# Performance work log

Measured on AMD Instinct MI355X. Metric: run time of the kernel, lower is better.

Reference implementation:

```python
import jax, jax.numpy as jnp
import numpy as np

N_T, N_M, E, Q = 100000, 20000, 600000, 200000
F_IN, D, L = 256, 128, 2


def setup_inputs() -> dict:
    key = jax.random.key(0)
    ks = jax.random.split(key, 20)
    s = 1.0 / np.sqrt(D)
    inp = {
        "x_thesis": jax.random.normal(ks[0], (N_T, F_IN), jnp.float32),
        "mentor_node_id": jnp.arange(N_M, dtype=jnp.int64) if jax.config.jax_enable_x64 else jnp.arange(N_M, dtype=jnp.int32),
        "edge_src": jax.random.randint(ks[1], (E,), 0, N_T),
        "edge_dst": jax.random.randint(ks[2], (E,), 0, N_M),
        "eli_src": jax.random.randint(ks[3], (Q,), 0, N_T),
        "eli_dst": jax.random.randint(ks[4], (Q,), 0, N_M),
        # encoder params
        "thesis_lin_w": jax.random.normal(ks[5], (D, F_IN), jnp.float32) / np.sqrt(F_IN),
        "thesis_lin_b": jnp.zeros((D,), jnp.float32),
        "prof_emb": jax.random.normal(ks[6], (N_M, D), jnp.float32),
        # SAGEConv params per layer, per edge type (sup: thesis->mentor, rev: mentor->thesis)
        "W_nbr_sup": jax.random.normal(ks[7], (L, D, D), jnp.float32) * s,
        "W_root_sup": jax.random.normal(ks[8], (L, D, D), jnp.float32) * s,
        "b_sup": jnp.zeros((L, D), jnp.float32),
        "W_nbr_rev": jax.random.normal(ks[9], (L, D, D), jnp.float32) * s,
        "W_root_rev": jax.random.normal(ks[10], (L, D, D), jnp.float32) * s,
        "b_rev": jnp.zeros((L, D), jnp.float32),
        # classifier Linear(2*D -> 1)
        "cls_w": jax.random.normal(ks[11], (2 * D,), jnp.float32) * (1.0 / np.sqrt(2 * D)),
        "cls_b": jnp.zeros((), jnp.float32),
    }
    return inp


def reference(x_thesis, mentor_node_id, edge_src, edge_dst, eli_src, eli_dst,
              thesis_lin_w, thesis_lin_b, prof_emb,
              W_nbr_sup, W_root_sup, b_sup, W_nbr_rev, W_root_rev, b_rev,
              cls_w, cls_b):
    n_t = x_thesis.shape[0]
    n_m = prof_emb.shape[0]
    L_ = W_nbr_sup.shape[0]

    # node encoders
    h_t = x_thesis @ thesis_lin_w.T + thesis_lin_b          # [N_T, D]
    h_m = prof_emb[mentor_node_id]                          # [N_M, D]

    ones = jnp.ones(edge_src.shape[0], h_t.dtype)
    deg_m = jnp.maximum(jax.ops.segment_sum(ones, edge_dst, num_segments=n_m), 1.0)[:, None]
    deg_t = jnp.maximum(jax.ops.segment_sum(ones, edge_src, num_segments=n_t), 1.0)[:, None]

    for l in range(L_):
        # mean-aggregate thesis feats onto mentors (supervised_by edges)
        agg_m = jax.ops.segment_sum(h_t[edge_src], edge_dst, num_segments=n_m) / deg_m
        # mean-aggregate mentor feats onto theses (reverse edges)
        agg_t = jax.ops.segment_sum(h_m[edge_dst], edge_src, num_segments=n_t) / deg_t
        new_m = agg_m @ W_nbr_sup[l].T + h_m @ W_root_sup[l].T + b_sup[l]
        new_t = agg_t @ W_nbr_rev[l].T + h_t @ W_root_rev[l].T + b_rev[l]
        if l < L_ - 1:
            new_m = jax.nn.relu(new_m)
            new_t = jax.nn.relu(new_t)
        h_t, h_m = new_t, new_m

    # edge-level classifier: gather endpoints, concat, linear -> scalar per pair
    z = jnp.concatenate([h_t[eli_src], h_m[eli_dst]], axis=-1)  # [Q, 2D]
    return z @ cls_w + cls_b                                     # [Q]
```

## Files before the change

### kernel.cpp

```cpp
#include <hip/hip_runtime.h>
#include <cstdint>
#include <cstddef>

#define D 128
#define F_IN 256

typedef __attribute__((ext_vector_type(8))) short bf16x8;
typedef __attribute__((ext_vector_type(4))) float f32x4;

__device__ __forceinline__ unsigned short f2bs(float f) {
  unsigned int x = __builtin_bit_cast(unsigned int, f);
  x = x + 0x7fffu + ((x >> 16) & 1u);
  return (unsigned short)(x >> 16);
}
__device__ __forceinline__ float b2f(unsigned int lo16) {
  unsigned int x = lo16 << 16;
  return __builtin_bit_cast(float, x);
}
__device__ __forceinline__ void gl_lds16v(const void* g, void* l) {
  __builtin_amdgcn_global_load_lds(
      (__attribute__((address_space(1))) void*)g,
      (__attribute__((address_space(3))) void*)l, 16, 0, 0);
}
__device__ __forceinline__ uint4 pack8(float4 a, float4 b) {
  uint4 o;
  o.x = (unsigned)f2bs(a.x) | ((unsigned)f2bs(a.y) << 16);
  o.y = (unsigned)f2bs(a.z) | ((unsigned)f2bs(a.w) << 16);
  o.z = (unsigned)f2bs(b.x) | ((unsigned)f2bs(b.y) << 16);
  o.w = (unsigned)f2bs(b.z) | ((unsigned)f2bs(b.w) << 16);
  return o;
}


__global__ __launch_bounds__(256) void prep_k(
    const float* __restrict__ s0, unsigned short* __restrict__ d0, int n0,
    const float* __restrict__ s1, unsigned short* __restrict__ d1, int n1,
    const float* __restrict__ s2, unsigned short* __restrict__ d2, int n2,
    const float* __restrict__ s3, unsigned short* __restrict__ d3, int n3,
    const float* __restrict__ s4, unsigned short* __restrict__ d4, int n4,
    int nbC,
    const float* __restrict__ emb, const int* __restrict__ ids,
    unsigned short* __restrict__ hm, int NM, int nbG,
    const int* __restrict__ esrc, const int* __restrict__ edst,
    int* __restrict__ bktT, int* __restrict__ bktM,
    int E, int SHT, int SHM, int nbA)
{
  int bid = blockIdx.x;
  int tid = threadIdx.x;
  if (bid < nbC) {
    int j = bid * 256 + tid;
    const float* s; unsigned short* d;
    if (j < n0) { s = s0; d = d0; }
    else {
      j -= n0;
      if (j < n1) { s = s1; d = d1; }
      else {
        j -= n1;
        if (j < n2) { s = s2; d = d2; }
        else {
          j -= n2;
          if (j < n3) { s = s3; d = d3; }
          else { j -= n3; if (j >= n4) return; s = s4; d = d4; }
        }
      }
    }
    const float4* sp = (const float4*)(s + (size_t)j * 8);
    *(uint4*)(d + (size_t)j * 8) = pack8(sp[0], sp[1]);
    return;
  }
  bid -= nbC;
  if (bid < nbG) {
    int i = bid * 256 + tid;
    if (i >= NM * 16) return;
    int r = i >> 4, c = (i & 15) * 8;
    const float* s = emb + (size_t)ids[r] * D + c;
    *(uint4*)(hm + (size_t)r * D + c) = pack8(*(const float4*)s, *(const float4*)(s + 4));
    return;
  }
  bid -= nbG;
  __shared__ int sh[256];
  sh[tid] = 0;
  __syncthreads();
  int stride = nbA * 256;
  for (int e = bid * 256 + tid; e < E; e += stride) {
    atomicAdd(&sh[esrc[e] >> SHT], 1);
    atomicAdd(&sh[128 + (edst[e] >> SHM)], 1);
  }
  __syncthreads();
  if (tid < 128) { if (sh[tid]) atomicAdd(&bktT[tid], sh[tid]); }
  else { if (sh[tid]) atomicAdd(&bktM[tid - 128], sh[tid]); }
}


__global__ void a2_scan_k(const int* __restrict__ bktT, int* __restrict__ baseT, int* __restrict__ curT, int BT,
                          const int* __restrict__ bktM, int* __restrict__ baseM, int* __restrict__ curM, int BM) {
  __shared__ int sT[129], sM[129];
  int tid = threadIdx.x;
  if (tid < BT) sT[tid] = bktT[tid];
  if (tid < BM) sM[tid] = bktM[tid];
  __syncthreads();
  if (tid == 0) { int r = 0; for (int i = 0; i < BT; ++i) { int c = sT[i]; sT[i] = r; r += c; } sT[BT] = r; }
  if (tid == 1) { int r = 0; for (int i = 0; i < BM; ++i) { int c = sM[i]; sM[i] = r; r += c; } sM[BM] = r; }
  __syncthreads();
  if (tid <= BT) { baseT[tid] = sT[tid]; if (tid < BT) curT[tid] = sT[tid]; }
  if (tid <= BM) { baseM[tid] = sM[tid]; if (tid < BM) curM[tid] = sM[tid]; }
}


#define CH 4096

__global__ __launch_bounds__(256) void a3_part_k(
    const int* __restrict__ esrc, const int* __restrict__ edst,
    unsigned* __restrict__ partT, unsigned* __restrict__ partM,
    int* __restrict__ curT, int* __restrict__ curM,
    int E, int BT, int BM, int SHT, int SHM)
{
  __shared__ unsigned stT[CH], stM[CH];
  __shared__ int hT[128], lbT[128], lcT[128], gbT[128];
  __shared__ int hM[128], lbM[128], lcM[128], gbM[128];
  __shared__ int st2[256];
  int tid = threadIdx.x;
  int c0 = blockIdx.x * CH;
  int len = E - c0; if (len > CH) len = CH;

  if (tid < 128) { hT[tid] = 0; hM[tid] = 0; }
  __syncthreads();
  for (int i = tid; i < len; i += 256) {
    atomicAdd(&hT[esrc[c0 + i] >> SHT], 1);
    atomicAdd(&hM[edst[c0 + i] >> SHM], 1);
  }
  __syncthreads();
  int own = (tid < 128) ? hT[tid] : hM[tid - 128];
  st2[tid] = own;
  __syncthreads();
  for (int dd = 1; dd < 128; dd <<= 1) {
    int y = ((tid & 127) >= dd) ? st2[tid - dd] : 0;
    __syncthreads();
    st2[tid] += y;
    __syncthreads();
  }
  int excl = st2[tid] - own;
  if (tid < 128) { lbT[tid] = excl; lcT[tid] = excl; }
  else { lbM[tid - 128] = excl; lcM[tid - 128] = excl; }
  __syncthreads();
  if (tid < BT) { if (hT[tid]) gbT[tid] = atomicAdd(&curT[tid], hT[tid]); }
  if (tid >= 128 && tid - 128 < BM) { int m = tid - 128; if (hM[m]) gbM[m] = atomicAdd(&curM[m], hM[m]); }
  __syncthreads();
  for (int i = tid; i < len; i += 256) {
    unsigned s = (unsigned)esrc[c0 + i], dn = (unsigned)edst[c0 + i];
    int p = atomicAdd(&lcT[s >> SHT], 1);
    stT[p] = (s << 15) | dn;
    int q = atomicAdd(&lcM[dn >> SHM], 1);
    stM[q] = (dn << 17) | s;
  }
  __syncthreads();
  for (int b = 0; b < BT; ++b) {
    int cb = hT[b]; if (!cb) continue;
    int lb = lbT[b]; int gb = gbT[b];
    for (int i = tid; i < cb; i += 256) partT[gb + i] = stT[lb + i];
  }
  for (int b = 0; b < BM; ++b) {
    int cb = hM[b]; if (!cb) continue;
    int lb = lbM[b]; int gb = gbM[b];
    for (int i = tid; i < cb; i += 256) partM[gb + i] = stM[lb + i];
  }
}


#define BCAP 12288

__global__ __launch_bounds__(256) void b_csr_k(
    const unsigned* __restrict__ partT, const int* __restrict__ baseT,
    int* __restrict__ rowT, int* __restrict__ csrT, int NT, int BT, int SHT,
    const unsigned* __restrict__ partM, const int* __restrict__ baseM,
    int* __restrict__ rowM, int* __restrict__ csrM, int NM, int BM, int SHM, int E)
{
  __shared__ int cnt[1024];
  __shared__ int st[256];
  __shared__ unsigned stage[BCAP];

  const unsigned* part; const int* base; int* row; int* csr;
  int N, SH, KS; unsigned PM; int b; bool last;
  if ((int)blockIdx.x < BT) {
    part = partT; base = baseT; row = rowT; csr = csrT;
    N = NT; SH = SHT; KS = 15; PM = 0x7fffu; b = blockIdx.x; last = (b == BT - 1);
  } else {
    part = partM; base = baseM; row = rowM; csr = csrM;
    N = NM; SH = SHM; KS = 17; PM = 0x1ffffu; b = blockIdx.x - BT; last = (b == BM - 1);
  }
  int tid = threadIdx.x;
  int ebeg = base[b], eend = base[b + 1];
  int tot = eend - ebeg;
  int n0 = b << SH;
  int width = 1 << SH;
  int nw = N - n0; if (nw > width) nw = width;
  int seg = (width + 255) >> 8;

  for (int j = 0; j < seg; ++j) { int idx = tid * seg + j; if (idx < nw) cnt[idx] = 0; }
  __syncthreads();
  for (int i = tid; i < tot; i += 256) {
    int k = (int)(part[ebeg + i] >> KS) - n0;
    atomicAdd(&cnt[k], 1);
  }
  __syncthreads();
  int s = 0;
  for (int j = 0; j < seg; ++j) { int idx = tid * seg + j; if (idx < nw) s += cnt[idx]; }
  st[tid] = s;
  __syncthreads();
  for (int dd = 1; dd < 256; dd <<= 1) {
    int y = (tid >= dd) ? st[tid - dd] : 0;
    __syncthreads();
    st[tid] += y;
    __syncthreads();
  }
  int run = st[tid] - s;
  for (int j = 0; j < seg; ++j) {
    int idx = tid * seg + j;
    if (idx < nw) {
      int c = cnt[idx];
      row[n0 + idx] = ebeg + run;
      cnt[idx] = run;
      run += c;
    }
  }
  if (last && tid == 0) row[N] = E;
  __syncthreads();
  if (tot <= BCAP) {
    for (int i = tid; i < tot; i += 256) {
      unsigned p = part[ebeg + i];
      int k = (int)(p >> KS) - n0;
      int pos = atomicAdd(&cnt[k], 1);
      stage[pos] = p & PM;
    }
    __syncthreads();
    for (int i = tid; i < tot; i += 256) csr[ebeg + i] = (int)stage[i];
  } else {
    for (int i = tid; i < tot; i += 256) {
      unsigned p = part[ebeg + i];
      int k = (int)(p >> KS) - n0;
      int pos = atomicAdd(&cnt[k], 1);
      csr[ebeg + pos] = (int)(p & PM);
    }
  }
}


__global__ __launch_bounds__(256) void aggregate2_k(
    const unsigned short* __restrict__ tabM, const int* __restrict__ rowpM,
    const int* __restrict__ idxM, unsigned short* __restrict__ outM, int nM, int nblkM,
    const unsigned short* __restrict__ tabT, const int* __restrict__ rowpT,
    const int* __restrict__ idxT, unsigned short* __restrict__ outT, int nT)
{
  const unsigned short* tab; const int* rowp; const int* idx;
  unsigned short* outp; int n, nodeb;
  if ((int)blockIdx.x < nblkM) {
    tab = tabM; rowp = rowpM; idx = idxM; outp = outM; n = nM;
    nodeb = blockIdx.x * 8;
  } else {
    tab = tabT; rowp = rowpT; idx = idxT; outp = outT; n = nT;
    nodeb = (blockIdx.x - nblkM) * 8;
  }
  const int tid = threadIdx.x;
  const int l = tid & 63;
  const int l32 = l & 31;
  const int sub = l >> 5;
  const int node = nodeb + (tid >> 6) * 2 + sub;
  const int nodeC = node < n ? node : n - 1;
  int b = rowp[nodeC];
  int e = rowp[nodeC + 1];
  if (node >= n) e = b;
  const int deg = e - b;
  const int odeg = __shfl_xor(deg, 32, 64);
  const int trip = deg > odeg ? deg : odeg;
  const int qsafe = (e > b) ? (e - 1) : 0;
  const unsigned short* tl = tab + l32 * 4;
  float a0 = 0.f, a1 = 0.f, a2 = 0.f, a3 = 0.f;
  int k = 0;
  while (k + 8 <= trip) {
    int nn[8]; bool ok[8];
#pragma unroll
    for (int u = 0; u < 8; ++u) { int p = b + k + u; ok[u] = p < e; nn[u] = idx[ok[u] ? p : qsafe]; }
    uint2 vv[8];
#pragma unroll
    for (int u = 0; u < 8; ++u) { vv[u] = make_uint2(0u, 0u); if (ok[u]) vv[u] = *(const uint2*)(tl + (size_t)nn[u] * D); }
#pragma unroll
    for (int u = 0; u < 8; ++u) {
      a0 += b2f(vv[u].x & 0xffffu); a1 += b2f(vv[u].x >> 16);
      a2 += b2f(vv[u].y & 0xffffu); a3 += b2f(vv[u].y >> 16);
    }
    k += 8;
  }
  if (k + 4 <= trip) {
    int nn[4]; bool ok[4];
#pragma unroll
    for (int u = 0; u < 4; ++u) { int p = b + k + u; ok[u] = p < e; nn[u] = idx[ok[u] ? p : qsafe]; }
    uint2 vv[4];
#pragma unroll
    for (int u = 0; u < 4; ++u) { vv[u] = make_uint2(0u, 0u); if (ok[u]) vv[u] = *(const uint2*)(tl + (size_t)nn[u] * D); }
#pragma unroll
    for (int u = 0; u < 4; ++u) {
      a0 += b2f(vv[u].x & 0xffffu); a1 += b2f(vv[u].x >> 16);
      a2 += b2f(vv[u].y & 0xffffu); a3 += b2f(vv[u].y >> 16);
    }
    k += 4;
  }
  if (k < trip) {
    int nn[3]; bool ok[3];
#pragma unroll
    for (int u = 0; u < 3; ++u) { int p = b + k + u; ok[u] = p < e; nn[u] = idx[ok[u] ? p : qsafe]; }
    uint2 vv[3];
#pragma unroll
    for (int u = 0; u < 3; ++u) { vv[u] = make_uint2(0u, 0u); if (ok[u]) vv[u] = *(const uint2*)(tl + (size_t)nn[u] * D); }
#pragma unroll
    for (int u = 0; u < 3; ++u) {
      a0 += b2f(vv[u].x & 0xffffu); a1 += b2f(vv[u].x >> 16);
      a2 += b2f(vv[u].y & 0xffffu); a3 += b2f(vv[u].y >> 16);
    }
  }
  float inv = 1.0f / (float)(deg > 1 ? deg : 1);
  if (node < n) {
    uint2 o;
    o.x = (unsigned)f2bs(a0 * inv) | ((unsigned)f2bs(a1 * inv) << 16);
    o.y = (unsigned)f2bs(a2 * inv) | ((unsigned)f2bs(a3 * inv) << 16);
    *(uint2*)(outp + (size_t)node * D + l32 * 4) = o;
  }
}


template<bool RELU>
__device__ __forceinline__ void gemm_body(
    const unsigned short* __restrict__ Aop, const unsigned short* __restrict__ WA,
    const unsigned short* __restrict__ Bop, const unsigned short* __restrict__ WB,
    const float* __restrict__ bias, unsigned short* __restrict__ out, int M,
    int blk, char* smraw)
{
  unsigned short* bufA0 = (unsigned short*)smraw;
  unsigned short* bufW0 = (unsigned short*)(smraw + 16384);
  const int tid = threadIdx.x;
  const int w = tid >> 6, l = tid & 63;
  const int wr = w >> 1, wc = w & 1;
  const int lr = l & 15, kg = l >> 4;
  const int row0 = blk * 128;
  const int srow = l >> 2;
  const int su = l & 3;

  f32x4 acc[4][4] = {};

  auto stage = [&](int st, int bsel) {
    const unsigned short* Ap = (st < 4) ? Aop : Bop;
    const unsigned short* Wp = (st < 4) ? WA : WB;
    int k0 = (st & 3) * 32;
    unsigned short* bA = bufA0 + bsel * 4096;
    unsigned short* bW = bufW0 + bsel * 4096;
#pragma unroll
    for (int q = 0; q < 2; ++q) {
      int r = w * 32 + q * 16 + srow;
      int gr = row0 + r; if (gr >= M) gr = M - 1;
      int gu = su ^ ((r >> 1) & 3);
      gl_lds16v(Ap + (size_t)gr * D + k0 + gu * 8, bA + (w * 32 + q * 16) * 32 + l * 8);
      gl_lds16v(Wp + (size_t)r * D + k0 + gu * 8, bW + (w * 32 + q * 16) * 32 + l * 8);
    }
  };

  stage(0, 0);
#pragma unroll 1
  for (int st = 0; st < 8; ++st) {
    if (st < 7) {
      stage(st + 1, (st + 1) & 1);
      __builtin_amdgcn_sched_barrier(0);
      asm volatile("s_waitcnt vmcnt(4)" ::: "memory");
    } else {
      __builtin_amdgcn_sched_barrier(0);
      asm volatile("s_waitcnt vmcnt(0)" ::: "memory");
    }
    __builtin_amdgcn_s_barrier();
    __builtin_amdgcn_sched_barrier(0);
    const unsigned short* bA = bufA0 + (st & 1) * 4096;
    const unsigned short* bW = bufW0 + (st & 1) * 4096;
    bf16x8 aF[4], bF[4];
#pragma unroll
    for (int i = 0; i < 4; ++i) {
      int r = wr * 64 + i * 16 + lr;
      aF[i] = *(const bf16x8*)&bA[r * 32 + ((kg ^ ((r >> 1) & 3)) * 8)];
    }
#pragma unroll
    for (int j = 0; j < 4; ++j) {
      int r = wc * 64 + j * 16 + lr;
      bF[j] = *(const bf16x8*)&bW[r * 32 + ((kg ^ ((r >> 1) & 3)) * 8)];
    }
#pragma unroll
    for (int i = 0; i < 4; ++i)
#pragma unroll
      for (int j = 0; j < 4; ++j)
        acc[i][j] = __builtin_amdgcn_mfma_f32_16x16x32_bf16(aF[i], bF[j], acc[i][j], 0, 0, 0);
    __builtin_amdgcn_sched_barrier(0);
    __builtin_amdgcn_s_barrier();
  }

  __syncthreads();
  float bn[4];
#pragma unroll
  for (int j = 0; j < 4; ++j) bn[j] = bias[wc * 64 + j * 16 + lr];
  unsigned short* ow = (unsigned short*)smraw + w * 4096;
#pragma unroll
  for (int i = 0; i < 4; ++i)
#pragma unroll
    for (int j = 0; j < 4; ++j) {
      f32x4 v = acc[i][j];
#pragma unroll
      for (int r = 0; r < 4; ++r) {
        float x = v[r] + bn[j];
        if (RELU) x = fmaxf(x, 0.f);
        ow[(i * 16 + kg * 4 + r) * 64 + j * 16 + lr] = f2bs(x);
      }
    }
  __syncthreads();
#pragma unroll
  for (int q = 0; q < 8; ++q) {
    int u = q * 64 + l;
    int lrow = u >> 3;
    int cu = (u & 7) * 8;
    int gr = row0 + wr * 64 + lrow;
    if (gr < M)
      *(uint4*)(out + (size_t)gr * D + wc * 64 + cu) = *(const uint4*)&ow[lrow * 64 + cu];
  }
}

template<bool RELU>
__global__ __launch_bounds__(256) void gemm_pair_k(
    const unsigned short* __restrict__ Am, const unsigned short* __restrict__ WAm,
    const unsigned short* __restrict__ Bm, const unsigned short* __restrict__ WBm,
    const float* __restrict__ biasm, unsigned short* __restrict__ outm, int Mm, int nbm,
    const unsigned short* __restrict__ At, const unsigned short* __restrict__ WAt,
    const unsigned short* __restrict__ Bt, const unsigned short* __restrict__ WBt,
    const float* __restrict__ biast, unsigned short* __restrict__ outt, int Mt)
{
  __shared__ char smraw[32768];
  if ((int)blockIdx.x < nbm)
    gemm_body<RELU>(Am, WAm, Bm, WBm, biasm, outm, Mm, blockIdx.x, smraw);
  else
    gemm_body<RELU>(At, WAt, Bt, WBt, biast, outt, Mt, blockIdx.x - nbm, smraw);
}

__global__ __launch_bounds__(256) void gemm_enc_k(
    const float* __restrict__ A, const unsigned short* __restrict__ W,
    const float* __restrict__ bias, unsigned short* __restrict__ out, int M)
{
  __shared__ char smraw[49152];
  float* bufA0 = (float*)smraw;
  unsigned short* bufW0 = (unsigned short*)(smraw + 32768);
  const int tid = threadIdx.x;
  const int w = tid >> 6, l = tid & 63;
  const int wr = w >> 1, wc = w & 1;
  const int lr = l & 15, kg = l >> 4;
  const int row0 = blockIdx.x * 128;
  const int arow = l >> 3;
  const int au = l & 7;
  const int wrow = l >> 2;
  const int wu = l & 3;

  f32x4 acc[4][4] = {};

  auto stage = [&](int st, int bsel) {
    int k0 = st * 32;
    float* bA = bufA0 + bsel * 4096;
    unsigned short* bW = bufW0 + bsel * 4096;
#pragma unroll
    for (int q = 0; q < 4; ++q) {
      int r = w * 32 + q * 8 + arow;
      int gr = row0 + r; if (gr >= M) gr = M - 1;
      int gu = au ^ (r & 7);
      gl_lds16v(A + (size_t)gr * F_IN + k0 + gu * 4, bA + (w * 32 + q * 8) * 32 + l * 4);
    }
#pragma unroll
    for (int q = 0; q < 2; ++q) {
      int r = w * 32 + q * 16 + wrow;
      int gu = wu ^ ((r >> 1) & 3);
      gl_lds16v(W + (size_t)r * F_IN + k0 + gu * 8, bW + (w * 32 + q * 16) * 32 + l * 8);
    }
  };

  stage(0, 0);
#pragma unroll 1
  for (int st = 0; st < F_IN / 32; ++st) {
    if (st < F_IN / 32 - 1) {
      stage(st + 1, (st + 1) & 1);
      __builtin_amdgcn_sched_barrier(0);
      asm volatile("s_waitcnt vmcnt(6)" ::: "memory");
    } else {
      __builtin_amdgcn_sched_barrier(0);
      asm volatile("s_waitcnt vmcnt(0)" ::: "memory");
    }
    __builtin_amdgcn_s_barrier();
    __builtin_amdgcn_sched_barrier(0);
    const float* bA = bufA0 + (st & 1) * 4096;
    const unsigned short* bW = bufW0 + (st & 1) * 4096;
    bf16x8 aF[4], bF[4];
#pragma unroll
    for (int i = 0; i < 4; ++i) {
      int r = wr * 64 + i * 16 + lr;
      const float4* pa = (const float4*)(bA + r * 32);
      float4 v0 = pa[(2 * kg) ^ (r & 7)];
      float4 v1 = pa[(2 * kg + 1) ^ (r & 7)];
      uint4 c = pack8(v0, v1);
      aF[i] = *(bf16x8*)&c;
    }
#pragma unroll
    for (int j = 0; j < 4; ++j) {
      int r = wc * 64 + j * 16 + lr;
      bF[j] = *(const bf16x8*)&bW[r * 32 + ((kg ^ ((r >> 1) & 3)) * 8)];
    }
#pragma unroll
    for (int i = 0; i < 4; ++i)
#pragma unroll
      for (int j = 0; j < 4; ++j)
        acc[i][j] = __builtin_amdgcn_mfma_f32_16x16x32_bf16(aF[i], bF[j], acc[i][j], 0, 0, 0);
    __builtin_amdgcn_sched_barrier(0);
    __builtin_amdgcn_s_barrier();
  }

  __syncthreads();
  float bn[4];
#pragma unroll
  for (int j = 0; j < 4; ++j) bn[j] = bias[wc * 64 + j * 16 + lr];
  unsigned short* ow = (unsigned short*)smraw + w * 4096;
#pragma unroll
  for (int i = 0; i < 4; ++i)
#pragma unroll
    for (int j = 0; j < 4; ++j) {
      f32x4 v = acc[i][j];
#pragma unroll
      for (int r = 0; r < 4; ++r)
        ow[(i * 16 + kg * 4 + r) * 64 + j * 16 + lr] = f2bs(v[r] + bn[j]);
    }
  __syncthreads();
#pragma unroll
  for (int q = 0; q < 8; ++q) {
    int u = q * 64 + l;
    int lrow = u >> 3;
    int cu = (u & 7) * 8;
    int gr = row0 + wr * 64 + lrow;
    if (gr < M)
      *(uint4*)(out + (size_t)gr * D + wc * 64 + cu) = *(const uint4*)&ow[lrow * 64 + cu];
  }
}


__global__ __launch_bounds__(256) void classify_k(
    const unsigned short* __restrict__ ht, const unsigned short* __restrict__ hm,
    const int* __restrict__ qs, const int* __restrict__ qd,
    const float* __restrict__ w, const float* __restrict__ bptr,
    float* __restrict__ out, int Q)
{
  int g = blockIdx.x * 8 + (threadIdx.x >> 5);
  if (g >= Q) return;
  int l = threadIdx.x & 31;
  const unsigned short* src = (l < 16)
      ? ht + (size_t)qs[g] * D + l * 8
      : hm + (size_t)qd[g] * D + (l - 16) * 8;
  uint4 v = *(const uint4*)src;
  const float* wp = w + l * 8;
  float acc = 0.f;
  acc += b2f(v.x & 0xffffu) * wp[0];
  acc += b2f(v.x >> 16)     * wp[1];
  acc += b2f(v.y & 0xffffu) * wp[2];
  acc += b2f(v.y >> 16)     * wp[3];
  acc += b2f(v.z & 0xffffu) * wp[4];
  acc += b2f(v.z >> 16)     * wp[5];
  acc += b2f(v.w & 0xffffu) * wp[6];
  acc += b2f(v.w >> 16)     * wp[7];
#pragma unroll
  for (int m = 16; m >= 1; m >>= 1) acc += __shfl_xor(acc, m, 64);
  if (l == 0) out[g] = acc + bptr[0];
}


extern "C" void kernel_launch(void* const* d_in, const int* in_sizes, int n_in,
                              void* d_out, int out_size, void* d_ws, size_t ws_size,
                              hipStream_t stream)
{
  const float* x_thesis = (const float*)d_in[0];
  const int*   mentor_id = (const int*)d_in[1];
  const int*   esrc = (const int*)d_in[2];
  const int*   edst = (const int*)d_in[3];
  const int*   qsrc = (const int*)d_in[4];
  const int*   qdst = (const int*)d_in[5];
  const float* lin_w = (const float*)d_in[6];
  const float* lin_b = (const float*)d_in[7];
  const float* prof  = (const float*)d_in[8];
  const float* Wn_sup = (const float*)d_in[9];
  const float* Wr_sup = (const float*)d_in[10];
  const float* b_sup  = (const float*)d_in[11];
  const float* Wn_rev = (const float*)d_in[12];
  const float* Wr_rev = (const float*)d_in[13];
  const float* b_rev  = (const float*)d_in[14];
  const float* cls_w  = (const float*)d_in[15];
  const float* cls_b  = (const float*)d_in[16];

  const int NT = in_sizes[0] / F_IN;
  const int NM = in_sizes[1];
  const int E  = in_sizes[2];
  const int Q  = in_sizes[4];
  const int L  = in_sizes[11] / D;

  int SHT = 0; while ((((NT - 1) >> SHT) + 1) > 128) ++SHT;
  int SHM = 0; while ((((NM - 1) >> SHM) + 1) > 128) ++SHM;
  const int BT = ((NT - 1) >> SHT) + 1;
  const int BM = ((NM - 1) >> SHM) + 1;

  char* wsb = (char*)d_ws;
  size_t off = 0;
  auto alloc = [&](size_t bytes) {
    void* p = wsb + off;
    off = (off + bytes + 255) & ~(size_t)255;
    return p;
  };
  unsigned short* h_t   = (unsigned short*)alloc((size_t)NT * D * 2);
  unsigned short* a_t   = (unsigned short*)alloc((size_t)NT * D * 2);
  unsigned short* h_m   = (unsigned short*)alloc((size_t)NM * D * 2);
  unsigned short* a_m   = (unsigned short*)alloc((size_t)NM * D * 2);
  unsigned short* linw_bf = (unsigned short*)alloc((size_t)D * F_IN * 2);
  unsigned short* wns_bf  = (unsigned short*)alloc((size_t)L * D * D * 2);
  unsigned short* wrs_bf  = (unsigned short*)alloc((size_t)L * D * D * 2);
  unsigned short* wnr_bf  = (unsigned short*)alloc((size_t)L * D * D * 2);
  unsigned short* wrr_bf  = (unsigned short*)alloc((size_t)L * D * D * 2);
  int* row_t = (int*)alloc(((size_t)NT + 1) * 4);
  int* row_m = (int*)alloc(((size_t)NM + 1) * 4);
  int* csr_t = (int*)alloc((size_t)E * 4);
  int* csr_m = (int*)alloc((size_t)E * 4);
  unsigned* partT = (unsigned*)alloc((size_t)E * 4);
  unsigned* partM = (unsigned*)alloc((size_t)E * 4);
  size_t bkt_off = off;
  int* bktT  = (int*)alloc(128 * 4);
  int* bktM  = (int*)alloc(128 * 4);
  size_t bkt_end = off;
  int* baseT = (int*)alloc(129 * 4);
  int* baseM = (int*)alloc(129 * 4);
  int* curT  = (int*)alloc(128 * 4);
  int* curM  = (int*)alloc(128 * 4);
  (void)n_in; (void)out_size; (void)ws_size;

  (void)hipMemsetAsync(wsb + bkt_off, 0, bkt_end - bkt_off, stream);

  {
    int n0 = D * F_IN / 8, nw = L * D * D / 8;
    int totc = n0 + 4 * nw;
    int nbC = (totc + 255) / 256;
    int nbG = (NM * 16 + 255) / 256;
    int nbA = 256;
    prep_k<<<nbC + nbG + nbA, 256, 0, stream>>>(
        lin_w, linw_bf, n0, Wn_sup, wns_bf, nw, Wr_sup, wrs_bf, nw,
        Wn_rev, wnr_bf, nw, Wr_rev, wrr_bf, nw, nbC,
        prof, mentor_id, h_m, NM, nbG,
        esrc, edst, bktT, bktM, E, SHT, SHM, nbA);
  }
  a2_scan_k<<<1, 256, 0, stream>>>(bktT, baseT, curT, BT, bktM, baseM, curM, BM);
  a3_part_k<<<(E + CH - 1) / CH, 256, 0, stream>>>(
      esrc, edst, partT, partM, curT, curM, E, BT, BM, SHT, SHM);
  b_csr_k<<<BT + BM, 256, 0, stream>>>(
      partT, baseT, row_t, csr_t, NT, BT, SHT,
      partM, baseM, row_m, csr_m, NM, BM, SHM, E);

  gemm_enc_k<<<(NT + 127) / 128, 256, 0, stream>>>(x_thesis, linw_bf, lin_b, h_t, NT);

  int agg_nbm = (NM + 7) / 8, agg_nbt = (NT + 7) / 8;
  int gem_nbm = (NM + 127) / 128, gem_nbt = (NT + 127) / 128;
  for (int l = 0; l < L; ++l) {
    aggregate2_k<<<agg_nbm + agg_nbt, 256, 0, stream>>>(
        h_t, row_m, csr_m, a_m, NM, agg_nbm,
        h_m, row_t, csr_t, a_t, NT);

    const unsigned short* wns = wns_bf + (size_t)l * D * D;
    const unsigned short* wrs = wrs_bf + (size_t)l * D * D;
    const unsigned short* wnr = wnr_bf + (size_t)l * D * D;
    const unsigned short* wrr = wrr_bf + (size_t)l * D * D;
    const float* bs = b_sup + (size_t)l * D;
    const float* br = b_rev + (size_t)l * D;
    if (l < L - 1) {
      gemm_pair_k<true><<<gem_nbm + gem_nbt, 256, 0, stream>>>(
          a_m, wns, h_m, wrs, bs, a_m, NM, gem_nbm,
          a_t, wnr, h_t, wrr, br, a_t, NT);
    } else {
      gemm_pair_k<false><<<gem_nbm + gem_nbt, 256, 0, stream>>>(
          a_m, wns, h_m, wrs, bs, a_m, NM, gem_nbm,
          a_t, wnr, h_t, wrr, br, a_t, NT);
    }
    unsigned short* tmp;
    tmp = h_t; h_t = a_t; a_t = tmp;
    tmp = h_m; h_m = a_m; a_m = tmp;
  }

  classify_k<<<(Q + 7) / 8, 256, 0, stream>>>(h_t, h_m, qsrc, qdst, cls_w, cls_b,
                                              (float*)d_out, Q);
}
```

Before: 270.6 us.

## Fuse neighbor aggregation into per-layer SAGE GEMM kernel via LDS staging

Merges the separate aggregate kernel and the dual GEMM into one layer kernel. Each 64-row block first gathers and mean-reduces neighbor features into swizzled LDS, then runs the MFMA GEMM over the aggregate (from LDS) and the root features (streamed in). This removes the round trip of the aggregate through global memory and one launch per layer. In exchange the gather uses one 32-lane group per node, handled serially over 8 nodes, so per-node load-level parallelism drops. The GEMM also loses its double-buffered pipelining and the block tile shrinks to 64 rows.

```diff
diff --git a/kernel.cpp b/kernel.cpp
--- a/kernel.cpp
+++ b/kernel.cpp
@@ -13,6 +13,9 @@
   x = x + 0x7fffu + ((x >> 16) & 1u);
   return (unsigned short)(x >> 16);
 }
+__device__ __forceinline__ unsigned pk2(float lo, float hi) {
+  return (unsigned)f2bs(lo) | ((unsigned)f2bs(hi) << 16);
+}
 __device__ __forceinline__ float b2f(unsigned int lo16) {
   unsigned int x = lo16 << 16;
   return __builtin_bit_cast(float, x);
@@ -24,10 +27,8 @@
 }
 __device__ __forceinline__ uint4 pack8(float4 a, float4 b) {
   uint4 o;
-  o.x = (unsigned)f2bs(a.x) | ((unsigned)f2bs(a.y) << 16);
-  o.y = (unsigned)f2bs(a.z) | ((unsigned)f2bs(a.w) << 16);
-  o.z = (unsigned)f2bs(b.x) | ((unsigned)f2bs(b.y) << 16);
-  o.w = (unsigned)f2bs(b.z) | ((unsigned)f2bs(b.w) << 16);
+  o.x = pk2(a.x, a.y); o.y = pk2(a.z, a.w);
+  o.z = pk2(b.x, b.y); o.w = pk2(b.z, b.w);
   return o;
 }
 
@@ -245,165 +246,137 @@
 }
 
 
-__global__ __launch_bounds__(256) void aggregate2_k(
-    const unsigned short* __restrict__ tabM, const int* __restrict__ rowpM,
-    const int* __restrict__ idxM, unsigned short* __restrict__ outM, int nM, int nblkM,
-    const unsigned short* __restrict__ tabT, const int* __restrict__ rowpT,
-    const int* __restrict__ idxT, unsigned short* __restrict__ outT, int nT)
-{
-  const unsigned short* tab; const int* rowp; const int* idx;
-  unsigned short* outp; int n, nodeb;
-  if ((int)blockIdx.x < nblkM) {
-    tab = tabM; rowp = rowpM; idx = idxM; outp = outM; n = nM;
-    nodeb = blockIdx.x * 8;
-  } else {
-    tab = tabT; rowp = rowpT; idx = idxT; outp = outT; n = nT;
-    nodeb = (blockIdx.x - nblkM) * 8;
-  }
-  const int tid = threadIdx.x;
-  const int l = tid & 63;
-  const int l32 = l & 31;
-  const int sub = l >> 5;
-  const int node = nodeb + (tid >> 6) * 2 + sub;
-  const int nodeC = node < n ? node : n - 1;
-  int b = rowp[nodeC];
-  int e = rowp[nodeC + 1];
-  if (node >= n) e = b;
-  const int deg = e - b;
-  const int odeg = __shfl_xor(deg, 32, 64);
-  const int trip = deg > odeg ? deg : odeg;
-  const int qsafe = (e > b) ? (e - 1) : 0;
-  const unsigned short* tl = tab + l32 * 4;
-  float a0 = 0.f, a1 = 0.f, a2 = 0.f, a3 = 0.f;
-  int k = 0;
-  while (k + 8 <= trip) {
-    int nn[8]; bool ok[8];
-#pragma unroll
-    for (int u = 0; u < 8; ++u) { int p = b + k + u; ok[u] = p < e; nn[u] = idx[ok[u] ? p : qsafe]; }
-    uint2 vv[8];
-#pragma unroll
-    for (int u = 0; u < 8; ++u) { vv[u] = make_uint2(0u, 0u); if (ok[u]) vv[u] = *(const uint2*)(tl + (size_t)nn[u] * D); }
-#pragma unroll
-    for (int u = 0; u < 8; ++u) {
-      a0 += b2f(vv[u].x & 0xffffu); a1 += b2f(vv[u].x >> 16);
-      a2 += b2f(vv[u].y & 0xffffu); a3 += b2f(vv[u].y >> 16);
-    }
-    k += 8;
-  }
-  if (k + 4 <= trip) {
-    int nn[4]; bool ok[4];
-#pragma unroll
-    for (int u = 0; u < 4; ++u) { int p = b + k + u; ok[u] = p < e; nn[u] = idx[ok[u] ? p : qsafe]; }
-    uint2 vv[4];
-#pragma unroll
-    for (int u = 0; u < 4; ++u) { vv[u] = make_uint2(0u, 0u); if (ok[u]) vv[u] = *(const uint2*)(tl + (size_t)nn[u] * D); }
-#pragma unroll
-    for (int u = 0; u < 4; ++u) {
-      a0 += b2f(vv[u].x & 0xffffu); a1 += b2f(vv[u].x >> 16);
-      a2 += b2f(vv[u].y & 0xffffu); a3 += b2f(vv[u].y >> 16);
-    }
-    k += 4;
-  }
-  if (k < trip) {
-    int nn[3]; bool ok[3];
-#pragma unroll
-    for (int u = 0; u < 3; ++u) { int p = b + k + u; ok[u] = p < e; nn[u] = idx[ok[u] ? p : qsafe]; }
-    uint2 vv[3];
-#pragma unroll
-    for (int u = 0; u < 3; ++u) { vv[u] = make_uint2(0u, 0u); if (ok[u]) vv[u] = *(const uint2*)(tl + (size_t)nn[u] * D); }
-#pragma unroll
-    for (int u = 0; u < 3; ++u) {
-      a0 += b2f(vv[u].x & 0xffffu); a1 += b2f(vv[u].x >> 16);
-      a2 += b2f(vv[u].y & 0xffffu); a3 += b2f(vv[u].y >> 16);
-    }
-  }
-  float inv = 1.0f / (float)(deg > 1 ? deg : 1);
-  if (node < n) {
-    uint2 o;
-    o.x = (unsigned)f2bs(a0 * inv) | ((unsigned)f2bs(a1 * inv) << 16);
-    o.y = (unsigned)f2bs(a2 * inv) | ((unsigned)f2bs(a3 * inv) << 16);
-    *(uint2*)(outp + (size_t)node * D + l32 * 4) = o;
-  }
-}
-
-
 template<bool RELU>
-__device__ __forceinline__ void gemm_body(
-    const unsigned short* __restrict__ Aop, const unsigned short* __restrict__ WA,
-    const unsigned short* __restrict__ Bop, const unsigned short* __restrict__ WB,
-    const float* __restrict__ bias, unsigned short* __restrict__ out, int M,
-    int blk, char* smraw)
-{
-  unsigned short* bufA0 = (unsigned short*)smraw;
-  unsigned short* bufW0 = (unsigned short*)(smraw + 16384);
+__device__ __forceinline__ void layer_body(
+    const unsigned short* __restrict__ tab, const int* __restrict__ rowp,
+    const int* __restrict__ idx, const unsigned short* __restrict__ root,
+    const unsigned short* __restrict__ Wn, const unsigned short* __restrict__ Wr,
+    const float* __restrict__ bias, unsigned short* __restrict__ out,
+    int n, int blk, char* smraw)
+{
+  unsigned short* aggp = (unsigned short*)smraw;
+  unsigned short* wbuf = (unsigned short*)(smraw + 16384);
+  unsigned short* rbuf = (unsigned short*)(smraw + 24576);
   const int tid = threadIdx.x;
   const int w = tid >> 6, l = tid & 63;
+  const int g = tid >> 5;
+  const int l32 = tid & 31;
   const int wr = w >> 1, wc = w & 1;
   const int lr = l & 15, kg = l >> 4;
-  const int row0 = blk * 128;
-  const int srow = l >> 2;
-  const int su = l & 3;
-
-  f32x4 acc[4][4] = {};
-
-  auto stage = [&](int st, int bsel) {
-    const unsigned short* Ap = (st < 4) ? Aop : Bop;
-    const unsigned short* Wp = (st < 4) ? WA : WB;
-    int k0 = (st & 3) * 32;
-    unsigned short* bA = bufA0 + bsel * 4096;
-    unsigned short* bW = bufW0 + bsel * 4096;
-#pragma unroll
-    for (int q = 0; q < 2; ++q) {
-      int r = w * 32 + q * 16 + srow;
-      int gr = row0 + r; if (gr >= M) gr = M - 1;
-      int gu = su ^ ((r >> 1) & 3);
-      gl_lds16v(Ap + (size_t)gr * D + k0 + gu * 8, bA + (w * 32 + q * 16) * 32 + l * 8);
-      gl_lds16v(Wp + (size_t)r * D + k0 + gu * 8, bW + (w * 32 + q * 16) * 32 + l * 8);
-    }
-  };
-
-  stage(0, 0);
+  const int n0 = blk * 64;
+
+  const unsigned short* tl = tab + l32 * 4;
+  for (int i = 0; i < 8; ++i) {
+    int r = g * 8 + i;
+    int node = n0 + r;
+    int nodeC = node < n ? node : n - 1;
+    int b = rowp[nodeC];
+    int e = rowp[nodeC + 1];
+    if (node >= n) e = b;
+    int deg = e - b;
+    float a0 = 0.f, a1 = 0.f, a2 = 0.f, a3 = 0.f;
+    int p = b;
+    while (p + 8 <= e) {
+      int nn[8];
+#pragma unroll
+      for (int u = 0; u < 8; ++u) nn[u] = idx[p + u];
+      uint2 vv[8];
+#pragma unroll
+      for (int u = 0; u < 8; ++u) vv[u] = *(const uint2*)(tl + (size_t)nn[u] * D);
+#pragma unroll
+      for (int u = 0; u < 8; ++u) {
+        a0 += b2f(vv[u].x & 0xffffu); a1 += b2f(vv[u].x >> 16);
+        a2 += b2f(vv[u].y & 0xffffu); a3 += b2f(vv[u].y >> 16);
+      }
+      p += 8;
+    }
+    if (p + 4 <= e) {
+      int nn[4];
+#pragma unroll
+      for (int u = 0; u < 4; ++u) nn[u] = idx[p + u];
+      uint2 vv[4];
+#pragma unroll
+      for (int u = 0; u < 4; ++u) vv[u] = *(const uint2*)(tl + (size_t)nn[u] * D);
+#pragma unroll
+      for (int u = 0; u < 4; ++u) {
+        a0 += b2f(vv[u].x & 0xffffu); a1 += b2f(vv[u].x >> 16);
+        a2 += b2f(vv[u].y & 0xffffu); a3 += b2f(vv[u].y >> 16);
+      }
+      p += 4;
+    }
+    {
+      bool h0 = p < e, h1 = p + 1 < e, h2 = p + 2 < e;
+      int m0 = h0 ? idx[p] : 0, m1 = h1 ? idx[p + 1] : 0, m2 = h2 ? idx[p + 2] : 0;
+      uint2 w0 = make_uint2(0u, 0u), w1 = make_uint2(0u, 0u), w2 = make_uint2(0u, 0u);
+      if (h0) w0 = *(const uint2*)(tl + (size_t)m0 * D);
+      if (h1) w1 = *(const uint2*)(tl + (size_t)m1 * D);
+      if (h2) w2 = *(const uint2*)(tl + (size_t)m2 * D);
+      if (h0) { a0 += b2f(w0.x & 0xffffu); a1 += b2f(w0.x >> 16); a2 += b2f(w0.y & 0xffffu); a3 += b2f(w0.y >> 16); }
+      if (h1) { a0 += b2f(w1.x & 0xffffu); a1 += b2f(w1.x >> 16); a2 += b2f(w1.y & 0xffffu); a3 += b2f(w1.y >> 16); }
+      if (h2) { a0 += b2f(w2.x & 0xffffu); a1 += b2f(w2.x >> 16); a2 += b2f(w2.y & 0xffffu); a3 += b2f(w2.y >> 16); }
+    }
+    float inv = 1.0f / (float)(deg > 1 ? deg : 1);
+    int u = (l32 >> 1) ^ (r & 7);
+    *(uint2*)(aggp + r * 128 + u * 8 + (l32 & 1) * 4) =
+        make_uint2(pk2(a0 * inv, a1 * inv), pk2(a2 * inv, a3 * inv));
+  }
+  __syncthreads();
+
+  f32x4 acc[2][4] = {};
+  const int srow = l >> 2, su = l & 3;
 #pragma unroll 1
-  for (int st = 0; st < 8; ++st) {
-    if (st < 7) {
-      stage(st + 1, (st + 1) & 1);
-      __builtin_amdgcn_sched_barrier(0);
-      asm volatile("s_waitcnt vmcnt(4)" ::: "memory");
+  for (int ch = 0; ch < 8; ++ch) {
+    if (ch) __syncthreads();
+    {
+      const unsigned short* Wp = (ch < 4) ? Wn : Wr;
+      int k0 = (ch & 3) * 32;
+#pragma unroll
+      for (int q = 0; q < 2; ++q) {
+        int r = w * 32 + q * 16 + srow;
+        int gu = su ^ ((r >> 1) & 3);
+        gl_lds16v(Wp + (size_t)r * D + k0 + gu * 8, wbuf + (w * 32 + q * 16) * 32 + l * 8);
+      }
+      if (ch >= 4) {
+        int r = tid >> 2;
+        int gr = n0 + r; if (gr >= n) gr = n - 1;
+        int gu = su ^ ((r >> 1) & 3);
+        gl_lds16v(root + (size_t)gr * D + k0 + gu * 8, rbuf + r * 32 + su * 8);
+      }
+    }
+    __syncthreads();
+    bf16x8 aF[2], bF[4];
+    if (ch < 4) {
+#pragma unroll
+      for (int i = 0; i < 2; ++i) {
+        int rr = wr * 32 + i * 16 + lr;
+        int u = ((ch & 3) * 4 + kg) ^ (rr & 7);
+        aF[i] = *(const bf16x8*)&aggp[rr * 128 + u * 8];
+      }
     } else {
-      __builtin_amdgcn_sched_barrier(0);
-      asm volatile("s_waitcnt vmcnt(0)" ::: "memory");
-    }
-    __builtin_amdgcn_s_barrier();
-    __builtin_amdgcn_sched_barrier(0);
-    const unsigned short* bA = bufA0 + (st & 1) * 4096;
-    const unsigned short* bW = bufW0 + (st & 1) * 4096;
-    bf16x8 aF[4], bF[4];
-#pragma unroll
-    for (int i = 0; i < 4; ++i) {
-      int r = wr * 64 + i * 16 + lr;
-      aF[i] = *(const bf16x8*)&bA[r * 32 + ((kg ^ ((r >> 1) & 3)) * 8)];
+#pragma unroll
+      for (int i = 0; i < 2; ++i) {
+        int rr = wr * 32 + i * 16 + lr;
+        aF[i] = *(const bf16x8*)&rbuf[rr * 32 + ((kg ^ ((rr >> 1) & 3)) * 8)];
+      }
     }
 #pragma unroll
     for (int j = 0; j < 4; ++j) {
       int r = wc * 64 + j * 16 + lr;
-      bF[j] = *(const bf16x8*)&bW[r * 32 + ((kg ^ ((r >> 1) & 3)) * 8)];
-    }
-#pragma unroll
-    for (int i = 0; i < 4; ++i)
+      bF[j] = *(const bf16x8*)&wbuf[r * 32 + ((kg ^ ((r >> 1) & 3)) * 8)];
+    }
+#pragma unroll
+    for (int i = 0; i < 2; ++i)
 #pragma unroll
       for (int j = 0; j < 4; ++j)
         acc[i][j] = __builtin_amdgcn_mfma_f32_16x16x32_bf16(aF[i], bF[j], acc[i][j], 0, 0, 0);
-    __builtin_amdgcn_sched_barrier(0);
-    __builtin_amdgcn_s_barrier();
   }
 
   __syncthreads();
   float bn[4];
 #pragma unroll
   for (int j = 0; j < 4; ++j) bn[j] = bias[wc * 64 + j * 16 + lr];
-  unsigned short* ow = (unsigned short*)smraw + w * 4096;
-#pragma unroll
-  for (int i = 0; i < 4; ++i)
+#pragma unroll
+  for (int i = 0; i < 2; ++i)
 #pragma unroll
     for (int j = 0; j < 4; ++j) {
       f32x4 v = acc[i][j];
@@ -411,36 +384,39 @@
       for (int r = 0; r < 4; ++r) {
         float x = v[r] + bn[j];
         if (RELU) x = fmaxf(x, 0.f);
-        ow[(i * 16 + kg * 4 + r) * 64 + j * 16 + lr] = f2bs(x);
-      }
-    }
-  __syncthreads();
-#pragma unroll
-  for (int q = 0; q < 8; ++q) {
-    int u = q * 64 + l;
-    int lrow = u >> 3;
-    int cu = (u & 7) * 8;
-    int gr = row0 + wr * 64 + lrow;
-    if (gr < M)
-      *(uint4*)(out + (size_t)gr * D + wc * 64 + cu) = *(const uint4*)&ow[lrow * 64 + cu];
+        aggp[(wr * 32 + i * 16 + kg * 4 + r) * 128 + wc * 64 + j * 16 + lr] = f2bs(x);
+      }
+    }
+  __syncthreads();
+#pragma unroll
+  for (int q = 0; q < 4; ++q) {
+    int u = q * 256 + tid;
+    int lrow = u >> 4;
+    int cu = (u & 15) * 8;
+    int gr = n0 + lrow;
+    if (gr < n)
+      *(uint4*)(out + (size_t)gr * D + cu) = *(const uint4*)&aggp[lrow * 128 + cu];
   }
 }
 
 template<bool RELU>
-__global__ __launch_bounds__(256) void gemm_pair_k(
-    const unsigned short* __restrict__ Am, const unsigned short* __restrict__ WAm,
-    const unsigned short* __restrict__ Bm, const unsigned short* __restrict__ WBm,
-    const float* __restrict__ biasm, unsigned short* __restrict__ outm, int Mm, int nbm,
-    const unsigned short* __restrict__ At, const unsigned short* __restrict__ WAt,
-    const unsigned short* __restrict__ Bt, const unsigned short* __restrict__ WBt,
-    const float* __restrict__ biast, unsigned short* __restrict__ outt, int Mt)
-{
-  __shared__ char smraw[32768];
+__global__ __launch_bounds__(256) void layer_k(
+    const unsigned short* __restrict__ tabM, const int* __restrict__ rowpM,
+    const int* __restrict__ idxM, const unsigned short* __restrict__ rootM,
+    const unsigned short* __restrict__ WnM, const unsigned short* __restrict__ WrM,
+    const float* __restrict__ biasM, unsigned short* __restrict__ outM, int nM, int nbm,
+    const unsigned short* __restrict__ tabT, const int* __restrict__ rowpT,
+    const int* __restrict__ idxT, const unsigned short* __restrict__ rootT,
+    const unsigned short* __restrict__ WnT, const unsigned short* __restrict__ WrT,
+    const float* __restrict__ biasT, unsigned short* __restrict__ outT, int nT)
+{
+  __shared__ char smraw[28672];
   if ((int)blockIdx.x < nbm)
-    gemm_body<RELU>(Am, WAm, Bm, WBm, biasm, outm, Mm, blockIdx.x, smraw);
+    layer_body<RELU>(tabM, rowpM, idxM, rootM, WnM, WrM, biasM, outM, nM, blockIdx.x, smraw);
   else
-    gemm_body<RELU>(At, WAt, Bt, WBt, biast, outt, Mt, blockIdx.x - nbm, smraw);
-}
+    layer_body<RELU>(tabT, rowpT, idxT, rootT, WnT, WrT, biasT, outT, nT, blockIdx.x - nbm, smraw);
+}
+
 
 __global__ __launch_bounds__(256) void gemm_enc_k(
     const float* __restrict__ A, const unsigned short* __restrict__ W,
@@ -663,13 +639,8 @@
 
   gemm_enc_k<<<(NT + 127) / 128, 256, 0, stream>>>(x_thesis, linw_bf, lin_b, h_t, NT);
 
-  int agg_nbm = (NM + 7) / 8, agg_nbt = (NT + 7) / 8;
-  int gem_nbm = (NM + 127) / 128, gem_nbt = (NT + 127) / 128;
+  int nbm64 = (NM + 63) / 64, nbt64 = (NT + 63) / 64;
   for (int l = 0; l < L; ++l) {
-    aggregate2_k<<<agg_nbm + agg_nbt, 256, 0, stream>>>(
-        h_t, row_m, csr_m, a_m, NM, agg_nbm,
-        h_m, row_t, csr_t, a_t, NT);
-
     const unsigned short* wns = wns_bf + (size_t)l * D * D;
     const unsigned short* wrs = wrs_bf + (size_t)l * D * D;
     const unsigned short* wnr = wnr_bf + (size_t)l * D * D;
@@ -677,13 +648,13 @@
     const float* bs = b_sup + (size_t)l * D;
     const float* br = b_rev + (size_t)l * D;
     if (l < L - 1) {
-      gemm_pair_k<true><<<gem_nbm + gem_nbt, 256, 0, stream>>>(
-          a_m, wns, h_m, wrs, bs, a_m, NM, gem_nbm,
-          a_t, wnr, h_t, wrr, br, a_t, NT);
+      layer_k<true><<<nbm64 + nbt64, 256, 0, stream>>>(
+          h_t, row_m, csr_m, h_m, wns, wrs, bs, a_m, NM, nbm64,
+          h_m, row_t, csr_t, h_t, wnr, wrr, br, a_t, NT);
     } else {
-      gemm_pair_k<false><<<gem_nbm + gem_nbt, 256, 0, stream>>>(
-          a_m, wns, h_m, wrs, bs, a_m, NM, gem_nbm,
-          a_t, wnr, h_t, wrr, br, a_t, NT);
+      layer_k<false><<<nbm64 + nbt64, 256, 0, stream>>>(
+          h_t, row_m, csr_m, h_m, wns, wrs, bs, a_m, NM, nbm64,
+          h_m, row_t, csr_t, h_t, wnr, wrr, br, a_t, NT);
     }
     unsigned short* tmp;
     tmp = h_t; h_t = a_t; a_t = tmp;
```

Result: slower. 285.9 us (+5.7%).
